# Performance work log

Measured on AMD Instinct MI355X. Metric: run time of the kernel, lower is better.

## Reference

```python
import jax, jax.numpy as jnp
import numpy as np

HEADS = 16
LN_EPS = 1e-12
MINUS_INF = -10000.0  # matches DeepSpeed's minus_inf constant


def setup_inputs() -> dict:
    key = jax.random.key(0)
    ks = jax.random.split(key, 6)
    B, S, H = 2, 2048, 2048
    x = jax.random.normal(ks[0], (B, S, H), dtype=jnp.float32)
    mask = jnp.zeros((B, 1, 1, S), dtype=jnp.float32)  # additive float mask (no padding)
    qkvw = jax.random.normal(ks[1], (H, 3 * H), dtype=jnp.float32) * 0.02
    qkvb = jax.random.normal(ks[2], (3 * H,), dtype=jnp.float32) * 0.02
    ow = jax.random.normal(ks[3], (H, H), dtype=jnp.float32) * 0.02
    norm_w = jnp.ones((H,), dtype=jnp.float32)
    norm_b = jnp.zeros((H,), dtype=jnp.float32)
    return {"x": x, "mask": mask, "qkvw": qkvw, "qkvb": qkvb, "ow": ow,
            "norm_w": norm_w, "norm_b": norm_b}


def _layernorm(x, g, b):
    mu = jnp.mean(x, axis=-1, keepdims=True)
    var = jnp.mean(jnp.square(x - mu), axis=-1, keepdims=True)
    return (x - mu) * jax.lax.rsqrt(var + LN_EPS) * g + b


def reference(x, mask, qkvw, qkvb, ow, norm_w, norm_b):
    B, S, H = x.shape
    dh = H // HEADS
    # QKVGemmOp: fused layernorm + QKV projection
    inp_norm = _layernorm(x, norm_w, norm_b)                      # [B,S,H]
    qkv = jnp.einsum('bsh,he->bse', inp_norm, qkvw) + qkvb        # [B,S,3H]
    q, k, v = jnp.split(qkv, 3, axis=-1)
    q = q.reshape(B, S, HEADS, dh).transpose(0, 2, 1, 3)          # [B,Hd,S,dh]
    k = k.reshape(B, S, HEADS, dh).transpose(0, 2, 1, 3)
    v = v.reshape(B, S, HEADS, dh).transpose(0, 2, 1, 3)
    # SoftmaxContextOp: kernel scales q and k each by 1/norm_factor,
    # norm_factor = d_head**0.25 (use_mup=False) -> net scale 1/sqrt(d_head)
    scale = 1.0 / jnp.sqrt(jnp.asarray(dh, dtype=x.dtype))
    scores = jnp.einsum('bhqd,bhkd->bhqk', q, k) * scale          # [B,Hd,S,S]
    causal = jnp.tril(jnp.ones((S, S), dtype=bool))
    scores = jnp.where(causal[None, None], scores + mask, MINUS_INF)
    probs = jax.nn.softmax(scores, axis=-1)
    ctx = jnp.einsum('bhqk,bhkd->bhqd', probs, v)                 # [B,Hd,S,dh]
    ctx = ctx.transpose(0, 2, 1, 3).reshape(B, S, H)
    # VectorMatMulOp: output projection (no bias here)
    out = jnp.einsum('bsh,ho->bso', ctx, ow)                      # [B,S,H]
    return (out, k, v, ctx, inp_norm)
```

## Files before the change

### kernel.cpp

```cpp
#include <hip/hip_runtime.h>

typedef short bf16x8 __attribute__((ext_vector_type(8)));
typedef float floatx4 __attribute__((ext_vector_type(4)));

#define MFMA16(a, b, c) __builtin_amdgcn_mfma_f32_16x16x32_bf16((a), (b), (c), 0, 0, 0)

__device__ __forceinline__ unsigned short f2bf(float f) {
    union { float f; unsigned int u; } v; v.f = f;
    unsigned int u = v.u;
    return (unsigned short)((u + 0x7FFFu + ((u >> 16) & 1u)) >> 16);
}

__device__ __forceinline__ void gld_lds16(const void* g, void* l) {
    __builtin_amdgcn_global_load_lds(
        (const __attribute__((address_space(1))) unsigned int*)g,
        (__attribute__((address_space(3))) unsigned int*)l, 16, 0, 0);
}

__global__ __launch_bounds__(256) void ln_kernel(
        const float* __restrict__ x, const float* __restrict__ g,
        const float* __restrict__ be, float* __restrict__ yo,
        unsigned short* __restrict__ yb) {
    int row = blockIdx.x, t = threadIdx.x;
    const float* xr = x + (size_t)row * 2048;
    float4 a = ((const float4*)xr)[2 * t];
    float4 b = ((const float4*)xr)[2 * t + 1];
    float s = a.x + a.y + a.z + a.w + b.x + b.y + b.z + b.w;
    float q = a.x * a.x + a.y * a.y + a.z * a.z + a.w * a.w +
              b.x * b.x + b.y * b.y + b.z * b.z + b.w * b.w;
    for (int m = 1; m < 64; m <<= 1) { s += __shfl_xor(s, m); q += __shfl_xor(q, m); }
    __shared__ float red[8];
    if ((t & 63) == 0) { red[t >> 6] = s; red[4 + (t >> 6)] = q; }
    __syncthreads();
    s = red[0] + red[1] + red[2] + red[3];
    q = red[4] + red[5] + red[6] + red[7];
    float mean = s * (1.0f / 2048.0f);
    float var = q * (1.0f / 2048.0f) - mean * mean;
    float rs = rsqrtf(var + 1e-12f);
    float4 g0 = ((const float4*)g)[2 * t], g1 = ((const float4*)g)[2 * t + 1];
    float4 b0 = ((const float4*)be)[2 * t], b1 = ((const float4*)be)[2 * t + 1];
    float4 y0, y1;
    y0.x = (a.x - mean) * rs * g0.x + b0.x;
    y0.y = (a.y - mean) * rs * g0.y + b0.y;
    y0.z = (a.z - mean) * rs * g0.z + b0.z;
    y0.w = (a.w - mean) * rs * g0.w + b0.w;
    y1.x = (b.x - mean) * rs * g1.x + b1.x;
    y1.y = (b.y - mean) * rs * g1.y + b1.y;
    y1.z = (b.z - mean) * rs * g1.z + b1.z;
    y1.w = (b.w - mean) * rs * g1.w + b1.w;
    float* yr = yo + (size_t)row * 2048;
    ((float4*)yr)[2 * t] = y0;
    ((float4*)yr)[2 * t + 1] = y1;
    union { unsigned short u[8]; uint4 v; } pk;
    pk.u[0] = f2bf(y0.x); pk.u[1] = f2bf(y0.y); pk.u[2] = f2bf(y0.z); pk.u[3] = f2bf(y0.w);
    pk.u[4] = f2bf(y1.x); pk.u[5] = f2bf(y1.y); pk.u[6] = f2bf(y1.z); pk.u[7] = f2bf(y1.w);
    *(uint4*)(yb + (size_t)row * 2048 + t * 8) = pk.v;
}

__global__ __launch_bounds__(256) void transpose_cvt(
        const float* __restrict__ src, unsigned short* __restrict__ dst,
        int K, int N) {
    __shared__ unsigned short tile[64][73];
    int n0 = blockIdx.x * 64, k0 = blockIdx.y * 64;
    size_t bo = (size_t)blockIdx.z * K * N;
    int t = threadIdx.x;
    for (int p = 0; p < 4; p++) {
        int idx = p * 256 + t; int r = idx >> 4; int c = (idx & 15) * 4;
        float4 v = *(const float4*)(src + bo + (size_t)(k0 + r) * N + n0 + c);
        tile[r][c] = f2bf(v.x); tile[r][c + 1] = f2bf(v.y);
        tile[r][c + 2] = f2bf(v.z); tile[r][c + 3] = f2bf(v.w);
    }
    __syncthreads();
    for (int p = 0; p < 4; p++) {
        int idx = p * 256 + t; int n = idx >> 4; int c = (idx & 15) * 4;
        ushort4 o;
        o.x = tile[c][n]; o.y = tile[c + 1][n];
        o.z = tile[c + 2][n]; o.w = tile[c + 3][n];
        *(ushort4*)(dst + bo + (size_t)(n0 + n) * K + k0 + c) = o;
    }
}

#define NT_QKV 32

__device__ __forceinline__ void stage_A(const unsigned short* __restrict__ Ag,
        unsigned short* As, int mh, int m0, int kt, int tid) {
#pragma unroll
    for (int j = 0; j < 2; j++) {
        int G = j * 512 + tid;
        int s = (G >> 3) & 63;
        int gr = G & 7;
        int row = j * 128 + mh * 64 + s;
        const unsigned short* src =
            Ag + (size_t)(m0 + row) * 2048 + kt * 64 + ((gr ^ (s & 7)) << 3);
        unsigned short* dst = As + j * 8192 + mh * 4096 + (tid >> 6) * 512;
        gld_lds16(src, dst);
    }
}

__device__ __forceinline__ void stage_B(const unsigned short* __restrict__ Bg,
        unsigned short* Bs, int nh, int n0, int kt, int tid) {
#pragma unroll
    for (int j = 0; j < 2; j++) {
        int G = j * 512 + tid;
        int wcc = G >> 8;
        int s = (G >> 3) & 31;
        int gr = G & 7;
        int row = wcc * 64 + nh * 32 + s;
        const unsigned short* src =
            Bg + (size_t)(n0 + row) * 2048 + kt * 64 + ((gr ^ (s & 7)) << 3);
        unsigned short* dst = Bs + wcc * 4096 + nh * 2048 + ((tid >> 6) & 3) * 512;
        gld_lds16(src, dst);
    }
}

__device__ __forceinline__ bf16x8 ldfrag(const unsigned short* S, int row, int ks,
                                         int quad, int ln15) {
    int gr = ((ks << 2) | quad) ^ (ln15 & 7);
    return *(const bf16x8*)(S + row * 64 + gr * 8);
}

#define PHASE_SYNC()                                        \
    __builtin_amdgcn_s_barrier();                           \
    asm volatile("s_waitcnt lgkmcnt(0)" ::: "memory");      \
    __builtin_amdgcn_sched_barrier(0);                      \
    __builtin_amdgcn_s_setprio(1)

#define PHASE_END()                                         \
    __builtin_amdgcn_s_setprio(0);                          \
    asm volatile("s_waitcnt vmcnt(4)" ::: "memory");        \
    __builtin_amdgcn_s_barrier()

__device__ __forceinline__ void qkv_tile(
        const unsigned short* __restrict__ Ag, const unsigned short* __restrict__ Bg,
        unsigned short* Asc, unsigned short* Bsc,
        unsigned short* Asn, unsigned short* Bsn,
        int t, int m0, int n0, int tid, int wr, int wc, int ln15, int quad,
        floatx4 (&acc)[8][4]) {
    bf16x8 a[4][2], bb[2][2];
    bool pf = (t + 1 < NT_QKV);
#pragma unroll
    for (int m = 0; m < 4; m++) {
        a[m][0] = ldfrag(Asc, wr * 128 + m * 16 + ln15, 0, quad, ln15);
        a[m][1] = ldfrag(Asc, wr * 128 + m * 16 + ln15, 1, quad, ln15);
    }
#pragma unroll
    for (int n = 0; n < 2; n++) {
        bb[n][0] = ldfrag(Bsc, wc * 64 + n * 16 + ln15, 0, quad, ln15);
        bb[n][1] = ldfrag(Bsc, wc * 64 + n * 16 + ln15, 1, quad, ln15);
    }
    if (pf) stage_B(Bg, Bsn, 0, n0, t + 1, tid);
    PHASE_SYNC();
#pragma unroll
    for (int m = 0; m < 4; m++)
#pragma unroll
        for (int n = 0; n < 2; n++) {
            acc[m][n] = MFMA16(a[m][0], bb[n][0], acc[m][n]);
            acc[m][n] = MFMA16(a[m][1], bb[n][1], acc[m][n]);
        }
    PHASE_END();
#pragma unroll
    for (int n = 0; n < 2; n++) {
        bb[n][0] = ldfrag(Bsc, wc * 64 + (2 + n) * 16 + ln15, 0, quad, ln15);
        bb[n][1] = ldfrag(Bsc, wc * 64 + (2 + n) * 16 + ln15, 1, quad, ln15);
    }
    if (pf) stage_A(Ag, Asn, 0, m0, t + 1, tid);
    PHASE_SYNC();
#pragma unroll
    for (int m = 0; m < 4; m++)
#pragma unroll
        for (int n = 0; n < 2; n++) {
            acc[m][2 + n] = MFMA16(a[m][0], bb[n][0], acc[m][2 + n]);
            acc[m][2 + n] = MFMA16(a[m][1], bb[n][1], acc[m][2 + n]);
        }
    PHASE_END();
#pragma unroll
    for (int m = 0; m < 4; m++) {
        a[m][0] = ldfrag(Asc, wr * 128 + (4 + m) * 16 + ln15, 0, quad, ln15);
        a[m][1] = ldfrag(Asc, wr * 128 + (4 + m) * 16 + ln15, 1, quad, ln15);
    }
    if (pf) stage_B(Bg, Bsn, 1, n0, t + 1, tid);
    PHASE_SYNC();
#pragma unroll
    for (int m = 0; m < 4; m++)
#pragma unroll
        for (int n = 0; n < 2; n++) {
            acc[4 + m][2 + n] = MFMA16(a[m][0], bb[n][0], acc[4 + m][2 + n]);
            acc[4 + m][2 + n] = MFMA16(a[m][1], bb[n][1], acc[4 + m][2 + n]);
        }
    PHASE_END();
#pragma unroll
    for (int n = 0; n < 2; n++) {
        bb[n][0] = ldfrag(Bsc, wc * 64 + n * 16 + ln15, 0, quad, ln15);
        bb[n][1] = ldfrag(Bsc, wc * 64 + n * 16 + ln15, 1, quad, ln15);
    }
    if (pf) stage_A(Ag, Asn, 1, m0, t + 1, tid);
    PHASE_SYNC();
#pragma unroll
    for (int m = 0; m < 4; m++)
#pragma unroll
        for (int n = 0; n < 2; n++) {
            acc[4 + m][n] = MFMA16(a[m][0], bb[n][0], acc[4 + m][n]);
            acc[4 + m][n] = MFMA16(a[m][1], bb[n][1], acc[4 + m][n]);
        }
    PHASE_END();
}

__global__ __launch_bounds__(512, 2) void gemm_qkv(
        const unsigned short* __restrict__ A, const unsigned short* __restrict__ Bt,
        const float* __restrict__ bias, float* __restrict__ ko,
        float* __restrict__ vo, unsigned short* __restrict__ qws,
        unsigned short* __restrict__ kbf) {
    __shared__ __align__(16) unsigned short As[2][16384];
    __shared__ __align__(16) unsigned short Bs[2][16384];
    int bid = blockIdx.x;
    int xcd = bid & 7, idx = bid >> 3;
    int mt = (xcd & 3) * 4 + idx / 12;
    int ntile = (xcd >> 2) * 12 + idx % 12;
    int m0 = mt * 256, n0 = ntile * 256;
    int tid = threadIdx.x;
    int wave = tid >> 6, lane = tid & 63, ln15 = lane & 15, quad = lane >> 4;
    int wr = wave >> 2, wc = wave & 3;
    floatx4 acc[8][4] = {};
    stage_B(Bt, Bs[0], 0, n0, 0, tid);
    stage_A(A, As[0], 0, m0, 0, tid);
    stage_B(Bt, Bs[0], 1, n0, 0, tid);
    stage_A(A, As[0], 1, m0, 0, tid);
    asm volatile("s_waitcnt vmcnt(4)" ::: "memory");
    __builtin_amdgcn_s_barrier();
#pragma unroll 1
    for (int t = 0; t < NT_QKV; t += 2) {
        qkv_tile(A, Bt, As[0], Bs[0], As[1], Bs[1], t,     m0, n0, tid, wr, wc, ln15, quad, acc);
        qkv_tile(A, Bt, As[1], Bs[1], As[0], Bs[0], t + 1, m0, n0, tid, wr, wc, ln15, quad, acc);
    }
#pragma unroll
    for (int mi = 0; mi < 8; mi++) {
        int row = m0 + wr * 128 + mi * 16 + quad * 4;
#pragma unroll
        for (int ni = 0; ni < 4; ni++) {
            int col = n0 + wc * 64 + ni * 16 + ln15;
            float bv = bias[col];
#pragma unroll
            for (int r = 0; r < 4; r++) {
                float val = acc[mi][ni][r] + bv;
                int rr = row + r;
                int b = rr >> 11, s = rr & 2047;
                if (col < 2048) {
                    qws[(size_t)rr * 2048 + col] = f2bf(val);
                } else if (col < 4096) {
                    int cc = col - 2048; int h = cc >> 7, d = cc & 127;
                    size_t o = ((size_t)(b * 16 + h) * 2048 + s) * 128 + d;
                    ko[o] = val;
                    kbf[o] = f2bf(val);
                } else {
                    int cc = col - 4096; int h = cc >> 7, d = cc & 127;
                    vo[((size_t)(b * 16 + h) * 2048 + s) * 128 + d] = val;
                }
            }
        }
    }
}

__global__ __launch_bounds__(256) void gemm_out(
        const float* __restrict__ Actx, const unsigned short* __restrict__ Bt,
        float* __restrict__ out) {
    __shared__ unsigned short As[128 * 72];
    __shared__ unsigned short Bs[128 * 72];
    int m0 = blockIdx.y * 128, n0 = blockIdx.x * 128;
    int t = threadIdx.x;
    int wave = t >> 6, lane = t & 63, ln15 = lane & 15, quad = lane >> 4;
    int wm = wave >> 1, wn = wave & 1;
    floatx4 acc[4][4] = {};
    for (int k0 = 0; k0 < 2048; k0 += 64) {
        for (int p = 0; p < 4; p++) {
            int idx = p * 256 + t; int r = idx >> 3; int c = (idx & 7) * 8;
            const float* ap = Actx + (size_t)(m0 + r) * 2048 + k0 + c;
            float4 u0 = ((const float4*)ap)[0], u1 = ((const float4*)ap)[1];
            union { unsigned short u[8]; uint4 v; } pk;
            pk.u[0] = f2bf(u0.x); pk.u[1] = f2bf(u0.y); pk.u[2] = f2bf(u0.z); pk.u[3] = f2bf(u0.w);
            pk.u[4] = f2bf(u1.x); pk.u[5] = f2bf(u1.y); pk.u[6] = f2bf(u1.z); pk.u[7] = f2bf(u1.w);
            *(uint4*)&As[r * 72 + c] = pk.v;
            *(uint4*)&Bs[r * 72 + c] = *(const uint4*)(Bt + (size_t)(n0 + r) * 2048 + k0 + c);
        }
        __syncthreads();
        for (int ks = 0; ks < 2; ks++) {
            bf16x8 af[4], bfr[4];
            for (int i = 0; i < 4; i++)
                af[i] = *(const bf16x8*)&As[(wm * 64 + i * 16 + ln15) * 72 + ks * 32 + quad * 8];
            for (int i = 0; i < 4; i++)
                bfr[i] = *(const bf16x8*)&Bs[(wn * 64 + i * 16 + ln15) * 72 + ks * 32 + quad * 8];
            for (int mi = 0; mi < 4; mi++)
                for (int ni = 0; ni < 4; ni++)
                    acc[mi][ni] = MFMA16(af[mi], bfr[ni], acc[mi][ni]);
        }
        __syncthreads();
    }
    for (int mi = 0; mi < 4; mi++) {
        int row = m0 + wm * 64 + mi * 16 + quad * 4;
        for (int ni = 0; ni < 4; ni++) {
            int col = n0 + wn * 64 + ni * 16 + ln15;
            for (int r = 0; r < 4; r++)
                out[(size_t)(row + r) * 2048 + col] = acc[mi][ni][r];
        }
    }
}

__device__ __forceinline__ void load_kv(const unsigned short* __restrict__ kb,
                                        const unsigned short* __restrict__ vTb,
                                        int c0, int t, uint4 (&kg)[4], uint4 (&vg)[4]) {
#pragma unroll
    for (int p = 0; p < 4; p++) {
        int idx = p * 256 + t;
        int r = idx >> 4, c = (idx & 15) * 8;
        kg[p] = *(const uint4*)(kb + (size_t)(c0 + r) * 128 + c);
        int d = idx >> 3, sg = (idx & 7) * 8;
        vg[p] = *(const uint4*)(vTb + (size_t)d * 2048 + c0 + sg);
    }
}

__global__ __launch_bounds__(256, 2) void attn_kernel(
        const unsigned short* __restrict__ qws, const unsigned short* __restrict__ kbf,
        const unsigned short* __restrict__ vT, const float* __restrict__ mask,
        float* __restrict__ ctxo) {
    __shared__ unsigned short Ks[64 * 136];
    __shared__ unsigned short Vt[128 * 72];
    __shared__ unsigned short Pl[4 * 16 * 72];
    int jp = blockIdx.x, h = blockIdx.y, b = blockIdx.z;
    int t = threadIdx.x, wave = t >> 6, lane = t & 63, ln15 = lane & 15, quad = lane >> 4;
    const float scale = 0.08838834764831845f;

    const unsigned short* kb = kbf + (size_t)(b * 16 + h) * 2048 * 128;
    const unsigned short* vTb = vT + (size_t)(b * 16 + h) * 128 * 2048;
    const float* mb = mask + (size_t)b * 2048;

    uint4 kg[4], vg[4];
    load_kv(kb, vTb, 0, t, kg, vg);

#pragma unroll 1
    for (int half = 0; half < 2; half++) {
        int qt = half ? (31 - jp) : jp;
        int Q0 = qt * 64;

        bf16x8 qf[4];
        const unsigned short* qbase =
            qws + ((size_t)(b * 2048 + Q0 + wave * 16 + ln15)) * 2048 + h * 128;
#pragma unroll
        for (int ks = 0; ks < 4; ks++)
            qf[ks] = *(const bf16x8*)(qbase + ks * 32 + quad * 8);

        float m_r[4], l_r[4];
        floatx4 o[8] = {};
#pragma unroll
        for (int r = 0; r < 4; r++) { m_r[r] = -1e30f; l_r[r] = 0.0f; }

        int nkt = qt + 1;
#pragma unroll 1
        for (int kt = 0; kt < nkt; kt++) {
            int c0 = kt * 64;
#pragma unroll
            for (int p = 0; p < 4; p++) {
                int idx = p * 256 + t;
                int r = idx >> 4, c = (idx & 15) * 8;
                *(uint4*)&Ks[r * 136 + c] = kg[p];
                int d = idx >> 3, sg = (idx & 7) * 8;
                *(uint4*)&Vt[d * 72 + sg] = vg[p];
            }
            __syncthreads();
            if (kt + 1 < nkt)      load_kv(kb, vTb, c0 + 64, t, kg, vg);
            else if (half == 0)    load_kv(kb, vTb, 0, t, kg, vg);

            floatx4 cs[4] = {};
            __builtin_amdgcn_s_setprio(1);
#pragma unroll
            for (int ks = 0; ks < 4; ks++)
#pragma unroll
                for (int ni = 0; ni < 4; ni++) {
                    bf16x8 kfr = *(const bf16x8*)&Ks[(ni * 16 + ln15) * 136 + ks * 32 + quad * 8];
                    cs[ni] = MFMA16(qf[ks], kfr, cs[ni]);
                }
            __builtin_amdgcn_s_setprio(0);

            float sv[4][4];
            float mt[4] = {-1e30f, -1e30f, -1e30f, -1e30f};
            if (kt == qt) {
#pragma unroll
                for (int ni = 0; ni < 4; ni++) {
                    int cg = c0 + ni * 16 + ln15;
                    float mk = mb[cg];
#pragma unroll
                    for (int r = 0; r < 4; r++) {
                        int qg = Q0 + wave * 16 + quad * 4 + r;
                        float v = (cg <= qg) ? fmaf(cs[ni][r], scale, mk) : -10000.0f;
                        sv[ni][r] = v;
                        mt[r] = fmaxf(mt[r], v);
                    }
                }
            } else {
#pragma unroll
                for (int ni = 0; ni < 4; ni++) {
                    float mk = mb[c0 + ni * 16 + ln15];
#pragma unroll
                    for (int r = 0; r < 4; r++) {
                        float v = fmaf(cs[ni][r], scale, mk);
                        sv[ni][r] = v;
                        mt[r] = fmaxf(mt[r], v);
                    }
                }
            }
#pragma unroll
            for (int m = 1; m < 16; m <<= 1)
#pragma unroll
                for (int r = 0; r < 4; r++) mt[r] = fmaxf(mt[r], __shfl_xor(mt[r], m));

            bool grow = false;
#pragma unroll
            for (int r = 0; r < 4; r++) grow = grow || (mt[r] > m_r[r] + 8.0f);
            if (__any((int)grow)) {
#pragma unroll
                for (int r = 0; r < 4; r++) {
                    float mn = fmaxf(m_r[r], mt[r]);
                    float al = __expf(m_r[r] - mn);
                    m_r[r] = mn;
                    l_r[r] *= al;
#pragma unroll
                    for (int nj = 0; nj < 8; nj++) o[nj][r] *= al;
                }
            }

            float lt[4] = {0.0f, 0.0f, 0.0f, 0.0f};
#pragma unroll
            for (int ni = 0; ni < 4; ni++)
#pragma unroll
                for (int r = 0; r < 4; r++) {
                    float p = __expf(sv[ni][r] - m_r[r]);
                    sv[ni][r] = p;
                    lt[r] += p;
                }
#pragma unroll
            for (int m = 1; m < 16; m <<= 1)
#pragma unroll
                for (int r = 0; r < 4; r++) lt[r] += __shfl_xor(lt[r], m);
#pragma unroll
            for (int r = 0; r < 4; r++) l_r[r] += lt[r];

            unsigned short* pw = &Pl[wave * 16 * 72];
#pragma unroll
            for (int ni = 0; ni < 4; ni++)
#pragma unroll
                for (int r = 0; r < 4; r++)
                    pw[(quad * 4 + r) * 72 + ni * 16 + ln15] = f2bf(sv[ni][r]);

            __builtin_amdgcn_s_setprio(1);
#pragma unroll
            for (int ks2 = 0; ks2 < 2; ks2++) {
                bf16x8 pf = *(const bf16x8*)&Pl[(wave * 16 + ln15) * 72 + ks2 * 32 + quad * 8];
#pragma unroll
                for (int nj = 0; nj < 8; nj++) {
                    bf16x8 vf = *(const bf16x8*)&Vt[(nj * 16 + ln15) * 72 + ks2 * 32 + quad * 8];
                    o[nj] = MFMA16(pf, vf, o[nj]);
                }
            }
            __builtin_amdgcn_s_setprio(0);
            __syncthreads();
        }

        float rl[4];
#pragma unroll
        for (int r = 0; r < 4; r++) rl[r] = 1.0f / l_r[r];
#pragma unroll
        for (int nj = 0; nj < 8; nj++)
#pragma unroll
            for (int r = 0; r < 4; r++) {
                int s = Q0 + wave * 16 + quad * 4 + r;
                ctxo[((size_t)(b * 2048 + s)) * 2048 + h * 128 + nj * 16 + ln15] = o[nj][r] * rl[r];
            }
    }
}

extern "C" void kernel_launch(void* const* d_in, const int* in_sizes, int n_in,
                              void* d_out, int out_size, void* d_ws, size_t ws_size,
                              hipStream_t stream) {
    const float* x      = (const float*)d_in[0];
    const float* mask   = (const float*)d_in[1];
    const float* qkvw   = (const float*)d_in[2];
    const float* qkvb   = (const float*)d_in[3];
    const float* ow     = (const float*)d_in[4];
    const float* norm_w = (const float*)d_in[5];
    const float* norm_b = (const float*)d_in[6];

    float* out      = (float*)d_out;
    float* k_out    = out + 8388608;
    float* v_out    = out + 16777216;
    float* ctx_out  = out + 25165824;
    float* norm_out = out + 33554432;

    unsigned short* ws    = (unsigned short*)d_ws;
    unsigned short* xn    = ws;
    unsigned short* qkvwT = ws + 8388608;
    unsigned short* owT   = ws + 8388608 + 12582912;
    unsigned short* qws   = owT + 4194304;
    unsigned short* vT    = qws + 8388608;
    unsigned short* kbf   = vT + 8388608;

    ln_kernel<<<4096, 256, 0, stream>>>(x, norm_w, norm_b, norm_out, xn);
    transpose_cvt<<<dim3(96, 32, 1), 256, 0, stream>>>(qkvw, qkvwT, 2048, 6144);
    transpose_cvt<<<dim3(32, 32, 1), 256, 0, stream>>>(ow, owT, 2048, 2048);
    gemm_qkv<<<dim3(384), 512, 0, stream>>>(xn, qkvwT, qkvb, k_out, v_out, qws, kbf);
    transpose_cvt<<<dim3(2, 32, 32), 256, 0, stream>>>(v_out, vT, 2048, 128);
    attn_kernel<<<dim3(16, 16, 2), 256, 0, stream>>>(qws, kbf, vT, mask, ctx_out);
    gemm_out<<<dim3(16, 32), 256, 0, stream>>>(ctx_out, owT, out);
}
```

Measured before the change: 650.3 us.

## Double-buffer K/V tiles in LDS via direct global-to-LDS loads with XOR swizzle

Replaces register-staged K/V prefetch with direct global_load_lds into a double-buffered LDS tile, synchronised with manual vmcnt waits and raw barriers. The padded layouts become unpadded tiles with an XOR swizzle on 16-byte chunks to avoid bank conflicts. The aim is to cut register pressure and the LDS store instructions, and to overlap the next tile's load with compute. It doubles the K/V LDS footprint, which may reduce occupancy at two blocks per CU. It also relies on correct vmcnt counting; the loads issued by the Q fragment path and the barriers without explicit LDS waits may cause ordering hazards.

```diff
diff --git a/kernel.cpp b/kernel.cpp
--- a/kernel.cpp
+++ b/kernel.cpp
@@ -304,16 +304,24 @@
     }
 }
 
-__device__ __forceinline__ void load_kv(const unsigned short* __restrict__ kb,
-                                        const unsigned short* __restrict__ vTb,
-                                        int c0, int t, uint4 (&kg)[4], uint4 (&vg)[4]) {
-#pragma unroll
-    for (int p = 0; p < 4; p++) {
-        int idx = p * 256 + t;
-        int r = idx >> 4, c = (idx & 15) * 8;
-        kg[p] = *(const uint4*)(kb + (size_t)(c0 + r) * 128 + c);
-        int d = idx >> 3, sg = (idx & 7) * 8;
-        vg[p] = *(const uint4*)(vTb + (size_t)d * 2048 + c0 + sg);
+__device__ __forceinline__ void stage_kv(const unsigned short* __restrict__ kb,
+                                         const unsigned short* __restrict__ vTb,
+                                         int c0, int tid,
+                                         unsigned short* KsB, unsigned short* VtB) {
+    int wb = (tid >> 6) << 6;
+#pragma unroll
+    for (int i = 0; i < 4; i++) {
+        int p = i * 256 + tid;
+        int r = p >> 4, s = p & 15;
+        int g = s ^ (r & 7);
+        gld_lds16(kb + (size_t)(c0 + r) * 128 + g * 8, KsB + (i * 256 + wb) * 8);
+    }
+#pragma unroll
+    for (int i = 0; i < 4; i++) {
+        int p = i * 256 + tid;
+        int d = p >> 3, s = p & 7;
+        int g = s ^ (d & 7);
+        gld_lds16(vTb + (size_t)d * 2048 + c0 + g * 8, VtB + (i * 256 + wb) * 8);
     }
 }
 
@@ -321,19 +329,20 @@
         const unsigned short* __restrict__ qws, const unsigned short* __restrict__ kbf,
         const unsigned short* __restrict__ vT, const float* __restrict__ mask,
         float* __restrict__ ctxo) {
-    __shared__ unsigned short Ks[64 * 136];
-    __shared__ unsigned short Vt[128 * 72];
+    __shared__ __align__(16) unsigned short Ks[2][64 * 128];
+    __shared__ __align__(16) unsigned short Vt[2][128 * 64];
     __shared__ unsigned short Pl[4 * 16 * 72];
     int jp = blockIdx.x, h = blockIdx.y, b = blockIdx.z;
     int t = threadIdx.x, wave = t >> 6, lane = t & 63, ln15 = lane & 15, quad = lane >> 4;
+    int x7 = ln15 & 7;
     const float scale = 0.08838834764831845f;
 
     const unsigned short* kb = kbf + (size_t)(b * 16 + h) * 2048 * 128;
     const unsigned short* vTb = vT + (size_t)(b * 16 + h) * 128 * 2048;
     const float* mb = mask + (size_t)b * 2048;
 
-    uint4 kg[4], vg[4];
-    load_kv(kb, vTb, 0, t, kg, vg);
+    int cur = 0;
+    stage_kv(kb, vTb, 0, t, Ks[0], Vt[0]);
 
 #pragma unroll 1
     for (int half = 0; half < 2; half++) {
@@ -356,17 +365,19 @@
 #pragma unroll 1
         for (int kt = 0; kt < nkt; kt++) {
             int c0 = kt * 64;
-#pragma unroll
-            for (int p = 0; p < 4; p++) {
-                int idx = p * 256 + t;
-                int r = idx >> 4, c = (idx & 15) * 8;
-                *(uint4*)&Ks[r * 136 + c] = kg[p];
-                int d = idx >> 3, sg = (idx & 7) * 8;
-                *(uint4*)&Vt[d * 72 + sg] = vg[p];
+            bool hn = true; int nc0 = 0;
+            if (kt + 1 < nkt)      nc0 = c0 + 64;
+            else if (half == 0)    nc0 = 0;
+            else                   hn = false;
+            if (hn) {
+                stage_kv(kb, vTb, nc0, t, Ks[cur ^ 1], Vt[cur ^ 1]);
+                asm volatile("s_waitcnt vmcnt(8)" ::: "memory");
+            } else {
+                asm volatile("s_waitcnt vmcnt(0)" ::: "memory");
             }
-            __syncthreads();
-            if (kt + 1 < nkt)      load_kv(kb, vTb, c0 + 64, t, kg, vg);
-            else if (half == 0)    load_kv(kb, vTb, 0, t, kg, vg);
+            __builtin_amdgcn_s_barrier();
+            const unsigned short* KsB = Ks[cur];
+            const unsigned short* VtB = Vt[cur];
 
             floatx4 cs[4] = {};
             __builtin_amdgcn_s_setprio(1);
@@ -374,7 +385,9 @@
             for (int ks = 0; ks < 4; ks++)
 #pragma unroll
                 for (int ni = 0; ni < 4; ni++) {
-                    bf16x8 kfr = *(const bf16x8*)&Ks[(ni * 16 + ln15) * 136 + ks * 32 + quad * 8];
+                    int rr = ni * 16 + ln15;
+                    int sl = (ks * 4 + quad) ^ x7;
+                    bf16x8 kfr = *(const bf16x8*)&KsB[rr * 128 + sl * 8];
                     cs[ni] = MFMA16(qf[ks], kfr, cs[ni]);
                 }
             __builtin_amdgcn_s_setprio(0);
@@ -455,12 +468,15 @@
                 bf16x8 pf = *(const bf16x8*)&Pl[(wave * 16 + ln15) * 72 + ks2 * 32 + quad * 8];
 #pragma unroll
                 for (int nj = 0; nj < 8; nj++) {
-                    bf16x8 vf = *(const bf16x8*)&Vt[(nj * 16 + ln15) * 72 + ks2 * 32 + quad * 8];
+                    int dd = nj * 16 + ln15;
+                    int sl = (ks2 * 4 + quad) ^ x7;
+                    bf16x8 vf = *(const bf16x8*)&VtB[dd * 64 + sl * 8];
                     o[nj] = MFMA16(pf, vf, o[nj]);
                 }
             }
             __builtin_amdgcn_s_setprio(0);
-            __syncthreads();
+            __builtin_amdgcn_s_barrier();
+            cur ^= 1;
         }
 
         float rl[4];
```

After: 550.6 us. 1.18x faster.
